# Performance work log

Measured on AMD Instinct MI355X. Metric: run time of the kernel, lower is better.

Reference implementation:

```python
import jax, jax.numpy as jnp
import numpy as np

D = 256          # input_dim
H = 4            # num_heads
W = 4            # window_size
NUM_SCALES = 3
FRACTAL = 2
NUM_CLASSES = 7


def _pool(t, ksize):
    # reflect-pad along time by ksize//2 each side, then avg_pool1d(kernel=stride=ksize)
    p = ksize // 2
    t = jnp.pad(t, ((0, 0), (p, p), (0, 0)), mode='reflect')
    B, Tp, F = t.shape
    L = Tp // ksize
    return t[:, :L * ksize].reshape(B, L, ksize, F).mean(axis=2)


def _window_attn(q, k, v):
    # windowed multi-head self-attention with zero-pad to a multiple of W
    B, T, F = q.shape
    pad = (-T) % W
    if pad:
        q = jnp.pad(q, ((0, 0), (0, pad), (0, 0)))
        k = jnp.pad(k, ((0, 0), (0, pad), (0, 0)))
        v = jnp.pad(v, ((0, 0), (0, pad), (0, 0)))
    Tp = T + pad
    nw = Tp // W
    hd = F // H
    scale = 1.0 / np.sqrt(hd).astype(np.float32)
    # [B, nw, W, H, hd] -> [B, nw, H, W, hd]
    qh = q.reshape(B, nw, W, H, hd).transpose(0, 1, 3, 2, 4)
    kh = k.reshape(B, nw, W, H, hd).transpose(0, 1, 3, 2, 4)
    vh = v.reshape(B, nw, W, H, hd).transpose(0, 1, 3, 2, 4)
    attn = jnp.einsum('bnhqd,bnhkd->bnhqk', qh, kh) * scale
    attn = jax.nn.softmax(attn, axis=-1)
    out = jnp.einsum('bnhqk,bnhkd->bnhqd', attn, vh)
    out = out.transpose(0, 1, 3, 2, 4).reshape(B, Tp, F)
    return out[:, :T]


def _upsample_nearest(f, out_len):
    # matches torch F.interpolate(mode='nearest'): src = floor(i * in / out)
    in_len = f.shape[1]
    idx = jnp.minimum((jnp.arange(out_len) * in_len) // out_len, in_len - 1)
    return f[:, idx]


def setup_inputs() -> dict:
    key = jax.random.key(0)
    ks = jax.random.split(key, 14)
    s = 1.0 / np.sqrt(D).astype(np.float32)
    inp = {
        'x': jax.random.normal(ks[0], (32, 4096, D), dtype=jnp.float32),
        'Wq': jax.random.normal(ks[1], (D, D), dtype=jnp.float32) * s,
        'bq': jnp.zeros((D,), jnp.float32),
        'Wk': jax.random.normal(ks[2], (D, D), dtype=jnp.float32) * s,
        'bk': jnp.zeros((D,), jnp.float32),
        'Wv': jax.random.normal(ks[3], (D, D), dtype=jnp.float32) * s,
        'bv': jnp.zeros((D,), jnp.float32),
        'Wp': jax.random.normal(ks[4], (D, D), dtype=jnp.float32) * s,
        'bp': jnp.zeros((D,), jnp.float32),
        'Wc1': jax.random.normal(ks[5], (D, D), dtype=jnp.float32) * s,
        'bc1': jnp.zeros((D,), jnp.float32),
        'Wc2': jax.random.normal(ks[6], (D, NUM_CLASSES), dtype=jnp.float32) * s,
        'bc2': jnp.zeros((NUM_CLASSES,), jnp.float32),
    }
    return inp


def reference(x, Wq, bq, Wk, bk, Wv, bv, Wp, bp, Wc1, bc1, Wc2, bc2):
    B, T, F = x.shape
    q = x @ Wq + bq
    k = x @ Wk + bk
    v = x @ Wv + bv
    # multi-scale temporal operator + per-scale fractal windowed attention
    outs = []
    for s_idx in range(1, NUM_SCALES + 1):
        ksize = FRACTAL ** (s_idx - 1)
        if ksize == 1:
            qs, ks_, vs = q, k, v
        else:
            qs, ks_, vs = _pool(q, ksize), _pool(k, ksize), _pool(v, ksize)
        outs.append(_window_attn(qs, ks_, vs))
    # scale mixer: nearest upsample + exact GELU + sum + proj
    summed = sum(jax.nn.gelu(_upsample_nearest(f, T), approximate=False) for f in outs)
    fused = summed @ Wp + bp
    # classifier (dropout inactive in eval)
    h = fused.mean(axis=1)
    h = jax.nn.relu(h @ Wc1 + bc1)
    logits = h @ Wc2 + bc2
    return logits
```

## Files before the change

kernel.cpp:

```cpp
#include <hip/hip_runtime.h>

#define DD 256
#define TT 4096
#define BB 32

typedef __attribute__((ext_vector_type(8))) short short8;
typedef __attribute__((ext_vector_type(4))) float floatx4;

__device__ __forceinline__ unsigned short f2bf(float f) {
    unsigned u = __builtin_bit_cast(unsigned, f);
    unsigned r = u + 0x7FFFu + ((u >> 16) & 1u);
    return (unsigned short)(r >> 16);
}
__device__ __forceinline__ float bf2f(unsigned short h) {
    return __builtin_bit_cast(float, (unsigned)h << 16);
}
__device__ __forceinline__ float2 unpk(unsigned u) {
    float2 r;
    r.x = __builtin_bit_cast(float, u << 16);
    r.y = __builtin_bit_cast(float, u & 0xFFFF0000u);
    return r;
}

#define GLDS16(g, l)                                                        \
    __builtin_amdgcn_global_load_lds(                                       \
        (const __attribute__((address_space(1))) void*)(g),                 \
        (__attribute__((address_space(3))) void*)(l), 16, 0, 0)

__global__ __launch_bounds__(256)
void prep_x_kernel(const float* __restrict__ X, unsigned short* __restrict__ Xh)
{
    size_t i = ((size_t)blockIdx.x * 256 + threadIdx.x) * 8;
    float4 a = *(const float4*)(X + i);
    float4 b = *(const float4*)(X + i + 4);
    short8 o;
    o[0] = (short)f2bf(a.x); o[1] = (short)f2bf(a.y);
    o[2] = (short)f2bf(a.z); o[3] = (short)f2bf(a.w);
    o[4] = (short)f2bf(b.x); o[5] = (short)f2bf(b.y);
    o[6] = (short)f2bf(b.z); o[7] = (short)f2bf(b.w);
    *(short8*)(Xh + i) = o;
}

__global__ void prep_w_kernel(const float* __restrict__ Wq,
                              const float* __restrict__ Wk,
                              const float* __restrict__ Wv,
                              unsigned short* __restrict__ Wt)
{
    const int z = blockIdx.y;
    const int k = blockIdx.x;
    const int n = threadIdx.x;
    const float* W = (z == 0) ? Wq : (z == 1) ? Wk : Wv;
    float w = W[k * 256 + n];
    unsigned short hi = f2bf(w);
    unsigned short lo = f2bf(w - bf2f(hi));
    size_t base = (size_t)z * 131072;
    Wt[base +         (size_t)n * 256 + k] = hi;
    Wt[base + 65536 + (size_t)n * 256 + k] = lo;
}

__global__ __launch_bounds__(256, 2)
void qkv_mfma_kernel(const unsigned short* __restrict__ Xh,
                     const unsigned short* __restrict__ Wt,
                     const float* __restrict__ bq, const float* __restrict__ bk,
                     const float* __restrict__ bv,
                     unsigned short* __restrict__ Q, unsigned short* __restrict__ Kp,
                     unsigned short* __restrict__ V)
{
    const int z = blockIdx.z;
    const unsigned short* Wz = Wt + (size_t)z * 131072;
    const float* bias = (z == 0) ? bq : (z == 1) ? bk : bv;
    unsigned short* Y = (z == 0) ? Q : (z == 1) ? Kp : V;

    __shared__ __align__(16) unsigned char smem[32768];
    unsigned short* Asm = (unsigned short*)smem;
    unsigned short* Bsm = (unsigned short*)(smem + 8192);

    const int tid = threadIdx.x;
    const int lane = tid & 63, wave = tid >> 6;
    const int wm = wave & 1, wn = wave >> 1;
    const int l15 = lane & 15, lq = lane >> 4;
    const int col0 = blockIdx.x * 128;
    const size_t row0 = (size_t)blockIdx.y * 128;

    floatx4 acc[4][4];
    #pragma unroll
    for (int i = 0; i < 4; ++i)
        #pragma unroll
        for (int j = 0; j < 4; ++j)
            acc[i][j] = (floatx4){0.f, 0.f, 0.f, 0.f};

    for (int k0 = 0; k0 < 256; k0 += 32) {
        __syncthreads();
        #pragma unroll
        for (int it = 0; it < 2; ++it) {
            int flat = it * 256 + tid;
            int m = flat >> 2, ks = (flat & 3) * 8;
            GLDS16(Xh + (row0 + m) * 256 + k0 + ks, Asm + flat * 8);
        }
        #pragma unroll
        for (int half = 0; half < 2; ++half)
            #pragma unroll
            for (int it = 0; it < 2; ++it) {
                int flat = it * 256 + tid;
                int n = flat >> 2, ks = (flat & 3) * 8;
                GLDS16(Wz + half * 65536 + (size_t)(col0 + n) * 256 + k0 + ks,
                       Bsm + half * 4096 + flat * 8);
            }
        __syncthreads();

        short8 a[4];
        #pragma unroll
        for (int mt = 0; mt < 4; ++mt)
            a[mt] = *(const short8*)(Asm + (wm * 64 + mt * 16 + l15) * 32 + lq * 8);
        #pragma unroll
        for (int nt = 0; nt < 4; ++nt) {
            const unsigned short* bp = Bsm + (wn * 64 + nt * 16 + l15) * 32 + lq * 8;
            short8 bh = *(const short8*)bp;
            short8 bl = *(const short8*)(bp + 4096);
            #pragma unroll
            for (int mt = 0; mt < 4; ++mt) {
                acc[mt][nt] = __builtin_amdgcn_mfma_f32_16x16x32_bf16(a[mt], bh, acc[mt][nt], 0, 0, 0);
                acc[mt][nt] = __builtin_amdgcn_mfma_f32_16x16x32_bf16(a[mt], bl, acc[mt][nt], 0, 0, 0);
            }
        }
    }

    __syncthreads();
    unsigned short* Cs = (unsigned short*)(smem + wave * 8192);
    #pragma unroll
    for (int nt = 0; nt < 4; ++nt) {
        float bv_ = bias[col0 + wn * 64 + nt * 16 + l15];
        #pragma unroll
        for (int mt = 0; mt < 4; ++mt)
            #pragma unroll
            for (int r = 0; r < 4; ++r) {
                int row = mt * 16 + lq * 4 + r;
                Cs[row * 64 + nt * 16 + l15] = f2bf(acc[mt][nt][r] + bv_);
            }
    }
    #pragma unroll
    for (int p = 0; p < 8; ++p) {
        int row = p * 8 + (lane >> 3);
        float4 d = *(const float4*)(Cs + row * 64 + (lane & 7) * 8);
        *(float4*)(Y + (row0 + wm * 64 + row) * 256 + col0 + wn * 64 + (lane & 7) * 8) = d;
    }
}

__device__ __forceinline__ float gelu_exact(float x) {
    return 0.5f * x * (1.0f + erff(x * 0.70710678118654752f));
}
__device__ __forceinline__ void addu4(uint4 d, float* f) {
    float2 t;
    t = unpk(d.x); f[0] += t.x; f[1] += t.y;
    t = unpk(d.y); f[2] += t.x; f[3] += t.y;
    t = unpk(d.z); f[4] += t.x; f[5] += t.y;
    t = unpk(d.w); f[6] += t.x; f[7] += t.y;
}

#define SPAN 32
#define NROW 34

template<int KS>
__device__ __forceinline__ void pool_qk(const unsigned short* __restrict__ qb,
                                        const unsigned short* __restrict__ kb,
                                        int rp,
                                        float* __restrict__ qf,
                                        float* __restrict__ kf)
{
    #pragma unroll
    for (int j = 0; j < KS; ++j) {
        int ra = (rp >> (8 * j)) & 0xFF;
        uint4 qd = *(const uint4*)(qb + ra * 256);
        uint4 kd = *(const uint4*)(kb + ra * 256);
        addu4(qd, qf);
        addu4(kd, kf);
    }
}

template<int KS>
__device__ __forceinline__ void pool_v(const unsigned short* __restrict__ vb,
                                       int rp, float* __restrict__ vf)
{
    #pragma unroll
    for (int j = 0; j < KS; ++j) {
        int ra = (rp >> (8 * j)) & 0xFF;
        uint4 vd = *(const uint4*)(vb + ra * 256);
        addu4(vd, vf);
    }
}

__global__ __launch_bounds__(256, 3)
void attn_fused_kernel(const unsigned short* __restrict__ Q,
                       const unsigned short* __restrict__ K,
                       const unsigned short* __restrict__ V,
                       float* __restrict__ acc)
{
    __shared__ __align__(16) unsigned char smem[3 * NROW * 256 * 2];
    unsigned short* qkvs = (unsigned short*)smem;
    float* scratch = (float*)smem;

    const int tid = threadIdx.x;
    const int s = blockIdx.x;
    const int b = blockIdx.y;
    const int r0 = s * SPAN;
    const int rbase = r0 - 2;

    #pragma unroll
    for (int t = 0; t < 3; ++t) {
        const unsigned short* src =
            ((t == 0) ? Q : (t == 1) ? K : V) + (size_t)b * TT * DD;
        #pragma unroll
        for (int it = 0; it < 5; ++it) {
            int flat = it * 256 + tid;
            if (flat < NROW * 32) {
                int row = flat >> 5, dc = flat & 31;
                int g = rbase + row;
                g = (g < 0) ? 0 : g;
                int c = (((dc >> 2) & 3) << 3) | ((dc & 3) << 1) | ((dc >> 4) & 1);
                GLDS16(src + (size_t)g * DD + c * 8,
                       qkvs + t * (NROW * 256) + flat * 8);
            }
        }
    }
    __syncthreads();

    const int slot = tid >> 2, lq = tid & 3;
    const int head = slot & 3, u = slot >> 2;
    int ksize, LEN, w; bool active = true;
    if (u < 8)       { ksize = 1; LEN = 4096; w = s * 8 + u; }
    else if (u < 12) { ksize = 2; LEN = 2049; w = s * 4 + (u - 8); }
    else if (u < 14) { ksize = 4; LEN = 1025; w = s * 2 + (u - 12); }
    else if (u == 14){ ksize = 2; LEN = 2049; w = 512; active = (s == 127); }
    else             { ksize = 4; LEN = 1025; w = 256; active = (s == 127); }

    const int f0 = head * 64 + lq * 16;
    const int fperm = head * 32 + lq * 8;

    float accL[16];
    #pragma unroll
    for (int e = 0; e < 16; ++e) accL[e] = 0.f;

    if (active) {
        int rp[4]; float cw[4]; int vmask = 0;
        for (int i = 0; i < 4; ++i) {
            int p = w * 4 + i;
            bool vv = (p < LEN);
            if (vv) vmask |= (1 << i);
            int pc = vv ? p : 0;
            int r[4] = {0, 0, 0, 0};
            if (ksize == 1) { r[0] = pc; }
            else if (ksize == 2) {
                if (pc == 0)            { r[0] = 0;      r[1] = 1;      }
                else if (pc == LEN - 1) { r[0] = TT - 2; r[1] = TT - 1; }
                else                    { r[0] = 2 * pc - 1; r[1] = 2 * pc; }
            } else {
                if (pc == 0)            { r[0] = 2; r[1] = 1; r[2] = 0; r[3] = 1; }
                else if (pc == LEN - 1) { r[0] = TT - 3; r[1] = TT - 2; r[2] = TT - 2; r[3] = TT - 1; }
                else                    { r[0] = 4*pc - 2; r[1] = 4*pc - 1; r[2] = 4*pc; r[3] = 4*pc + 1; }
            }
            int rr = 0;
            #pragma unroll
            for (int j = 0; j < 4; ++j) rr |= ((r[j] - rbase) & 0xFF) << (8 * j);
            rp[i] = rr;
            float c = 1.f;
            if (ksize != 1)
                c = (float)(((p + 1) * TT + LEN - 1) / LEN - (p * TT + LEN - 1) / LEN);
            cw[i] = vv ? c : 0.f;
        }
        const float inv_k = 1.0f / (float)ksize;
        const float sscale = 0.125f * inv_k * inv_k;

        float S[4][4];
        #pragma unroll
        for (int i = 0; i < 4; ++i)
            #pragma unroll
            for (int j = 0; j < 4; ++j) S[i][j] = 0.f;

        for (int half = 0; half < 2; ++half) {
            float qf[4][8], kf[4][8];
            const unsigned short* qb = qkvs + half * 128 + fperm;
            const unsigned short* kb = qb + NROW * 256;
            #pragma unroll
            for (int i = 0; i < 4; ++i) {
                #pragma unroll
                for (int e = 0; e < 8; ++e) { qf[i][e] = 0.f; kf[i][e] = 0.f; }
                if (vmask & (1 << i)) {
                    if (ksize == 1)      pool_qk<1>(qb, kb, rp[i], qf[i], kf[i]);
                    else if (ksize == 2) pool_qk<2>(qb, kb, rp[i], qf[i], kf[i]);
                    else                 pool_qk<4>(qb, kb, rp[i], qf[i], kf[i]);
                }
            }
            #pragma unroll
            for (int i = 0; i < 4; ++i)
                #pragma unroll
                for (int j = 0; j < 4; ++j) {
                    float d = 0.f;
                    #pragma unroll
                    for (int e = 0; e < 8; ++e) d = fmaf(qf[i][e], kf[j][e], d);
                    S[i][j] += d;
                }
        }
        #pragma unroll
        for (int i = 0; i < 4; ++i)
            #pragma unroll
            for (int j = 0; j < 4; ++j) {
                float t = S[i][j];
                t += __shfl_xor(t, 1, 64);
                t += __shfl_xor(t, 2, 64);
                S[i][j] = t * sscale;
            }
        float P[4][4];
        #pragma unroll
        for (int i = 0; i < 4; ++i) {
            float m = fmaxf(fmaxf(S[i][0], S[i][1]), fmaxf(S[i][2], S[i][3]));
            float e0 = __expf(S[i][0] - m), e1 = __expf(S[i][1] - m);
            float e2 = __expf(S[i][2] - m), e3 = __expf(S[i][3] - m);
            float inv = inv_k / (e0 + e1 + e2 + e3);
            P[i][0] = e0 * inv; P[i][1] = e1 * inv; P[i][2] = e2 * inv; P[i][3] = e3 * inv;
        }

        for (int half = 0; half < 2; ++half) {
            float vf[4][8];
            const unsigned short* vb = qkvs + 2 * NROW * 256 + half * 128 + fperm;
            #pragma unroll
            for (int i = 0; i < 4; ++i) {
                #pragma unroll
                for (int e = 0; e < 8; ++e) vf[i][e] = 0.f;
                if (vmask & (1 << i)) {
                    if (ksize == 1)      pool_v<1>(vb, rp[i], vf[i]);
                    else if (ksize == 2) pool_v<2>(vb, rp[i], vf[i]);
                    else                 pool_v<4>(vb, rp[i], vf[i]);
                }
            }
            #pragma unroll
            for (int i = 0; i < 4; ++i) {
                if (!(vmask & (1 << i))) continue;
                #pragma unroll
                for (int e = 0; e < 8; ++e) {
                    float o = P[i][0]*vf[0][e] + P[i][1]*vf[1][e]
                            + P[i][2]*vf[2][e] + P[i][3]*vf[3][e];
                    accL[half * 8 + e] += cw[i] * gelu_exact(o);
                }
            }
        }
    }

    __syncthreads();
    #pragma unroll
    for (int e = 0; e < 16; e += 4) {
        float4 d = {accL[e], accL[e+1], accL[e+2], accL[e+3]};
        *(float4*)(scratch + u * 256 + f0 + e) = d;
    }
    __syncthreads();
    float sum = 0.f;
    #pragma unroll
    for (int uu = 0; uu < 16; ++uu) sum += scratch[uu * 256 + tid];
    atomicAdd(&acc[b * DD + tid], sum);
}

__global__ __launch_bounds__(256)
void classifier_kernel(const float* __restrict__ acc,
                       const float* __restrict__ Wp,  const float* __restrict__ bp,
                       const float* __restrict__ Wc1, const float* __restrict__ bc1,
                       const float* __restrict__ Wc2, const float* __restrict__ bc2,
                       float* __restrict__ out)
{
    const int b = blockIdx.x;
    const int d = threadIdx.x;
    __shared__ float sm[256], sf[256], sh[256];

    sm[d] = acc[b * 256 + d] * (1.0f / 4096.0f);
    __syncthreads();

    float s = bp[d];
    for (int kk = 0; kk < 256; ++kk) s = fmaf(sm[kk], Wp[kk * 256 + d], s);
    sf[d] = s;
    __syncthreads();

    s = bc1[d];
    for (int kk = 0; kk < 256; ++kk) s = fmaf(sf[kk], Wc1[kk * 256 + d], s);
    sh[d] = fmaxf(s, 0.0f);
    __syncthreads();

    if (d < 7) {
        s = bc2[d];
        for (int kk = 0; kk < 256; ++kk) s = fmaf(sh[kk], Wc2[kk * 7 + d], s);
        out[b * 7 + d] = s;
    }
}

extern "C" void kernel_launch(void* const* d_in, const int* in_sizes, int n_in,
                              void* d_out, int out_size, void* d_ws, size_t ws_size,
                              hipStream_t stream)
{
    const float* x   = (const float*)d_in[0];
    const float* Wq  = (const float*)d_in[1];
    const float* bq  = (const float*)d_in[2];
    const float* Wk  = (const float*)d_in[3];
    const float* bk  = (const float*)d_in[4];
    const float* Wv  = (const float*)d_in[5];
    const float* bv  = (const float*)d_in[6];
    const float* Wp  = (const float*)d_in[7];
    const float* bp  = (const float*)d_in[8];
    const float* Wc1 = (const float*)d_in[9];
    const float* bc1 = (const float*)d_in[10];
    const float* Wc2 = (const float*)d_in[11];
    const float* bc2 = (const float*)d_in[12];
    float* out = (float*)d_out;

    const size_t plane = (size_t)BB * TT * DD;
    unsigned short* Q  = (unsigned short*)d_ws;
    unsigned short* K  = Q + plane;
    unsigned short* V  = K + plane;
    unsigned short* Xh = V + plane;
    unsigned short* Wt = Xh + plane;
    float* acc = (float*)(Wt + 3 * 131072);

    prep_x_kernel<<<dim3(16384), 256, 0, stream>>>(x, Xh);
    prep_w_kernel<<<dim3(256, 3), 256, 0, stream>>>(Wq, Wk, Wv, Wt);
    (void)hipMemsetAsync(acc, 0, BB * DD * sizeof(float), stream);

    qkv_mfma_kernel<<<dim3(2, 1024, 3), 256, 0, stream>>>(
        Xh, Wt, bq, bk, bv, Q, K, V);

    attn_fused_kernel<<<dim3(128, BB), 256, 0, stream>>>(Q, K, V, acc);

    classifier_kernel<<<dim3(BB), 256, 0, stream>>>(acc, Wp, bp, Wc1, bc1, Wc2, bc2, out);
}
```

Baseline: 473.4 us.

## Double-buffer QKV GEMM LDS tiles with k-panel layout and XOR swizzle

Moves X and the split-bf16 weights into a k-panel-major layout (32-wide K panels), so each GEMM stage reads contiguous 64-byte rows. The QKV MFMA kernel gains two LDS buffers: the next K-stage is issued with global_load_lds while the current stage is computed, which removes one barrier per iteration. An XOR swizzle on 16-byte chunks is meant to cut LDS bank conflicts on the fragment reads. LDS use rises to 48KB and the launch-bounds occupancy hint goes from 2 to 3 blocks. The loop relies on the single trailing barrier to order the async LDS writes, which is a correctness risk.

```diff
diff --git a/kernel.cpp b/kernel.cpp
--- a/kernel.cpp
+++ b/kernel.cpp
@@ -28,7 +28,7 @@
         (__attribute__((address_space(3))) void*)(l), 16, 0, 0)
 
 __global__ __launch_bounds__(256)
-void prep_x_kernel(const float* __restrict__ X, unsigned short* __restrict__ Xh)
+void prep_x_kernel(const float* __restrict__ X, unsigned short* __restrict__ Xp)
 {
     size_t i = ((size_t)blockIdx.x * 256 + threadIdx.x) * 8;
     float4 a = *(const float4*)(X + i);
@@ -38,7 +38,10 @@
     o[2] = (short)f2bf(a.z); o[3] = (short)f2bf(a.w);
     o[4] = (short)f2bf(b.x); o[5] = (short)f2bf(b.y);
     o[6] = (short)f2bf(b.z); o[7] = (short)f2bf(b.w);
-    *(short8*)(Xh + i) = o;
+    size_t row = i >> 8;
+    int k = (int)(i & 255);
+    size_t off = (size_t)(k >> 5) * (131072u * 32u) + row * 32 + (k & 31);
+    *(short8*)(Xp + off) = o;
 }
 
 __global__ void prep_w_kernel(const float* __restrict__ Wq,
@@ -54,12 +57,13 @@
     unsigned short hi = f2bf(w);
     unsigned short lo = f2bf(w - bf2f(hi));
     size_t base = (size_t)z * 131072;
-    Wt[base +         (size_t)n * 256 + k] = hi;
-    Wt[base + 65536 + (size_t)n * 256 + k] = lo;
-}
-
-__global__ __launch_bounds__(256, 2)
-void qkv_mfma_kernel(const unsigned short* __restrict__ Xh,
+    size_t off = (size_t)(k >> 5) * 8192 + (size_t)n * 32 + (k & 31);
+    Wt[base +         off] = hi;
+    Wt[base + 65536 + off] = lo;
+}
+
+__global__ __launch_bounds__(256, 3)
+void qkv_mfma_kernel(const unsigned short* __restrict__ Xp,
                      const unsigned short* __restrict__ Wt,
                      const float* __restrict__ bq, const float* __restrict__ bk,
                      const float* __restrict__ bv,
@@ -71,9 +75,7 @@
     const float* bias = (z == 0) ? bq : (z == 1) ? bk : bv;
     unsigned short* Y = (z == 0) ? Q : (z == 1) ? Kp : V;
 
-    __shared__ __align__(16) unsigned char smem[32768];
-    unsigned short* Asm = (unsigned short*)smem;
-    unsigned short* Bsm = (unsigned short*)(smem + 8192);
+    __shared__ __align__(16) unsigned char smem[49152];
 
     const int tid = threadIdx.x;
     const int lane = tid & 63, wave = tid >> 6;
@@ -89,32 +91,50 @@
         for (int j = 0; j < 4; ++j)
             acc[i][j] = (floatx4){0.f, 0.f, 0.f, 0.f};
 
-    for (int k0 = 0; k0 < 256; k0 += 32) {
-        __syncthreads();
+    auto stage = [&](int p, int pb) {
+        unsigned short* As = (unsigned short*)(smem + pb * 8192);
+        unsigned short* Bs = (unsigned short*)(smem + 16384 + pb * 16384);
+        const unsigned short* Ap = Xp + (size_t)p * (131072u * 32u);
+        const unsigned short* Bp = Wz + (size_t)p * 8192;
         #pragma unroll
         for (int it = 0; it < 2; ++it) {
             int flat = it * 256 + tid;
-            int m = flat >> 2, ks = (flat & 3) * 8;
-            GLDS16(Xh + (row0 + m) * 256 + k0 + ks, Asm + flat * 8);
+            int m = flat >> 2, c = flat & 3;
+            int sc = c ^ ((m >> 1) & 3);
+            GLDS16(Ap + (row0 + m) * 32 + sc * 8, As + flat * 8);
         }
         #pragma unroll
         for (int half = 0; half < 2; ++half)
             #pragma unroll
             for (int it = 0; it < 2; ++it) {
                 int flat = it * 256 + tid;
-                int n = flat >> 2, ks = (flat & 3) * 8;
-                GLDS16(Wz + half * 65536 + (size_t)(col0 + n) * 256 + k0 + ks,
-                       Bsm + half * 4096 + flat * 8);
-            }
-        __syncthreads();
+                int n = flat >> 2, c = flat & 3;
+                int sc = c ^ ((n >> 1) & 3);
+                GLDS16(Bp + half * 65536 + (size_t)(col0 + n) * 32 + sc * 8,
+                       Bs + half * 4096 + flat * 8);
+            }
+    };
+
+    stage(0, 0);
+    __syncthreads();
+
+    for (int k = 0; k < 8; ++k) {
+        const int pb = k & 1;
+        if (k < 7) stage(k + 1, pb ^ 1);
+
+        const unsigned short* As = (const unsigned short*)(smem + pb * 8192);
+        const unsigned short* Bs = (const unsigned short*)(smem + 16384 + pb * 16384);
 
         short8 a[4];
         #pragma unroll
-        for (int mt = 0; mt < 4; ++mt)
-            a[mt] = *(const short8*)(Asm + (wm * 64 + mt * 16 + l15) * 32 + lq * 8);
+        for (int mt = 0; mt < 4; ++mt) {
+            int row = wm * 64 + mt * 16 + l15;
+            a[mt] = *(const short8*)(As + row * 32 + (lq ^ ((row >> 1) & 3)) * 8);
+        }
         #pragma unroll
         for (int nt = 0; nt < 4; ++nt) {
-            const unsigned short* bp = Bsm + (wn * 64 + nt * 16 + l15) * 32 + lq * 8;
+            int nr = wn * 64 + nt * 16 + l15;
+            const unsigned short* bp = Bs + nr * 32 + (lq ^ ((nr >> 1) & 3)) * 8;
             short8 bh = *(const short8*)bp;
             short8 bl = *(const short8*)(bp + 4096);
             #pragma unroll
@@ -123,9 +143,9 @@
                 acc[mt][nt] = __builtin_amdgcn_mfma_f32_16x16x32_bf16(a[mt], bl, acc[mt][nt], 0, 0, 0);
             }
         }
-    }
-
-    __syncthreads();
+        __syncthreads();
+    }
+
     unsigned short* Cs = (unsigned short*)(smem + wave * 8192);
     #pragma unroll
     for (int nt = 0; nt < 4; ++nt) {
```

Measured after the change: 463.4 us. 2.1% less time.
